# Performance work log

Measured on AMD Instinct MI355X. Metric: run time of the kernel, lower is better.

Reference implementation:

```python
import jax, jax.numpy as jnp
import numpy as np

B, IN_DIM, HID, ODE_STEPS = 8192, 1024, 1024, 6
DT = 1.0


def setup_inputs() -> dict:
    key = jax.random.key(0)
    ks = jax.random.split(key, 8)
    s = 0.02  # init scale for stability
    return {
        "x": jax.random.normal(ks[0], (B, IN_DIM), dtype=jnp.float32),
        "h": jax.random.normal(ks[1], (B, HID), dtype=jnp.float32),
        "log_tau": jnp.zeros((HID,), dtype=jnp.float32),
        "W_in_w": jax.random.normal(ks[2], (HID, IN_DIM), dtype=jnp.float32) * s,
        "W_in_b": jnp.zeros((HID,), dtype=jnp.float32),
        "W_rec_w": jax.random.normal(ks[3], (HID, HID), dtype=jnp.float32) * s,
        "W_gate_w": jax.random.normal(ks[4], (HID, IN_DIM + HID), dtype=jnp.float32) * s,
        "W_gate_b": jnp.zeros((HID,), dtype=jnp.float32),
    }


def reference(x, h, log_tau, W_in_w, W_in_b, W_rec_w, W_gate_w, W_gate_b):
    # torch Linear: y = x @ W.T + b, W:(out,in)
    tau = jnp.exp(log_tau)                      # (HID,)
    input_drive = x @ W_in_w.T + W_in_b         # (B,HID), loop-invariant
    # W_gate acts on concat([x, h]); split into x-block and h-block.
    Wg_x = W_gate_w[:, :IN_DIM]
    Wg_h = W_gate_w[:, IN_DIM:]
    gate_x = x @ Wg_x.T + W_gate_b              # (B,HID), loop-invariant
    sub_dt = DT / ODE_STEPS
    scale = sub_dt / tau                        # (HID,)

    def step(h, _):
        gate = jax.nn.sigmoid(gate_x + h @ Wg_h.T)
        f = -h + gate * jnp.tanh(input_drive + h @ W_rec_w.T)
        return h + scale * f, None

    h, _ = jax.lax.scan(step, h, None, length=ODE_STEPS)
    return (h, h)
```

## Files before the change

### kernel.cpp

```cpp
#include <hip/hip_runtime.h>
#include <hip/hip_bf16.h>
#include <stdint.h>

#define B_DIM 8192
#define IN_DIMC 1024
#define HIDC 1024
#define K_DIM 1024
#define ODE_STEPS 6

typedef float f32x4 __attribute__((ext_vector_type(4)));
typedef short bf16x8 __attribute__((ext_vector_type(8)));
typedef unsigned short u16x8 __attribute__((ext_vector_type(8)));

__device__ __forceinline__ float bf2f(unsigned short u) {
    union { unsigned int u; float f; } c; c.u = ((unsigned int)u) << 16; return c.f;
}
__device__ __forceinline__ unsigned short f2bf(float f) {
    union { float f; unsigned int u; } c; c.f = f;
    unsigned int u = c.u;
    return (unsigned short)((u + 0x7fffu + ((u >> 16) & 1u)) >> 16);
}
__device__ __forceinline__ float fast_tanh(float x) {
    float e = __expf(2.0f * x);
    return 1.0f - 2.0f / (e + 1.0f);
}

constexpr size_t XN    = (size_t)B_DIM * IN_DIMC;
constexpr size_t HN    = (size_t)B_DIM * HIDC;
constexpr size_t WINN  = (size_t)HIDC * IN_DIMC;
constexpr size_t WRECN = (size_t)HIDC * HIDC;
constexpr size_t WGN   = (size_t)HIDC * (IN_DIMC + HIDC);
constexpr size_t TOTQ  = (XN + HN + WINN + WRECN + WGN) / 4;

__global__ __launch_bounds__(256) void convert_all(
    const float* __restrict__ x, const float* __restrict__ h,
    const float* __restrict__ win, const float* __restrict__ wrec,
    const float* __restrict__ wgate,
    unsigned short* __restrict__ x_bf, unsigned short* __restrict__ h_bf,
    unsigned short* __restrict__ win_bf, unsigned short* __restrict__ wrec_bf,
    unsigned short* __restrict__ wgx_bf, unsigned short* __restrict__ wgh_bf)
{
    size_t q = (size_t)blockIdx.x * 256 + threadIdx.x;
    if (q >= TOTQ) return;
    size_t e = q * 4;
    const float* src; unsigned short* dst; size_t si, di;
    if (e < XN)                          { src = x;    si = e;                       dst = x_bf;    di = si; }
    else if (e < XN + HN)                { src = h;    si = e - XN;                  dst = h_bf;    di = si; }
    else if (e < XN + HN + WINN)         { src = win;  si = e - XN - HN;             dst = win_bf;  di = si; }
    else if (e < XN + HN + WINN + WRECN) { src = wrec; si = e - XN - HN - WINN;      dst = wrec_bf; di = si; }
    else {
        size_t i = e - XN - HN - WINN - WRECN;
        size_t row = i >> 11, col = i & 2047;
        src = wgate; si = i;
        if (col < 1024) { dst = wgx_bf; di = row * 1024 + col; }
        else            { dst = wgh_bf; di = row * 1024 + (col - 1024); }
    }
    float4 v = *(const float4*)(src + si);
    ushort4 o;
    o.x = f2bf(v.x); o.y = f2bf(v.y); o.z = f2bf(v.z); o.w = f2bf(v.w);
    *(ushort4*)(dst + di) = o;
}

constexpr int BM = 128, BN = 64, BK = 32;
constexpr int NT = HIDC / BN;

__device__ __forceinline__ void gload_lds16(const void* g, void* l) {
    __builtin_amdgcn_global_load_lds(
        (const __attribute__((address_space(1))) void*)g,
        (__attribute__((address_space(3))) void*)l, 16, 0, 0);
}

template<bool STEP>
__global__ __launch_bounds__(256, 3) void ltc_gemm(
    const unsigned short* __restrict__ A,
    const unsigned short* __restrict__ B1,
    const unsigned short* __restrict__ B2,
    const unsigned short* __restrict__ GXID,
    const float* __restrict__ h_init,
    float* __restrict__ h_nat,
    const float* __restrict__ log_tau,
    float* __restrict__ h_out,
    float* __restrict__ h_out2,
    unsigned short* __restrict__ hbf_out,
    const float* __restrict__ bias1, const float* __restrict__ bias2,
    unsigned short* __restrict__ GXID_out)
{
    __shared__ __attribute__((aligned(16))) unsigned short lA[BM * BK];
    __shared__ __attribute__((aligned(16))) unsigned short lB1[BN * BK];
    __shared__ __attribute__((aligned(16))) unsigned short lB2[BN * BK];

    const int tid = threadIdx.x;
    const int w = tid >> 6, l = tid & 63;
    const int mt = blockIdx.x / NT, nt = blockIdx.x % NT;
    const int m0 = mt * BM, n0 = nt * BN;
    const int wm = (w >> 1) * 64, wn = (w & 1) * 32;
    const int lrow = l >> 2, lcol = (l & 3) * 8;
    const int lm = l & 15, lq = l >> 4;

    f32x4 acc1[4][2], acc2[4][2];
    f32x4 z4 = {0.f, 0.f, 0.f, 0.f};
    #pragma unroll
    for (int i = 0; i < 4; i++)
        #pragma unroll
        for (int j = 0; j < 2; j++) { acc1[i][j] = z4; acc2[i][j] = z4; }

    const int arow = w * 32;
    const unsigned short* Bsrc = (w < 2) ? B1 : B2;
    unsigned short* lBdst = (w < 2) ? lB1 : lB2;
    const int brow = (w & 1) * 32;

    for (int k0 = 0; k0 < K_DIM; k0 += BK) {
        #pragma unroll
        for (int i = 0; i < 2; i++) {
            int ra = arow + i * 16;
            int rb = brow + i * 16;
            gload_lds16(A    + (size_t)(m0 + ra + lrow) * K_DIM + k0 + lcol, &lA[ra * BK]);
            gload_lds16(Bsrc + (size_t)(n0 + rb + lrow) * K_DIM + k0 + lcol, &lBdst[rb * BK]);
        }
        __syncthreads();

        bf16x8 af[4], f1[2], f2[2];
        #pragma unroll
        for (int mi = 0; mi < 4; mi++)
            af[mi] = *(const bf16x8*)&lA[(wm + mi * 16 + lm) * BK + lq * 8];
        #pragma unroll
        for (int ni = 0; ni < 2; ni++) {
            f1[ni] = *(const bf16x8*)&lB1[(wn + ni * 16 + lm) * BK + lq * 8];
            f2[ni] = *(const bf16x8*)&lB2[(wn + ni * 16 + lm) * BK + lq * 8];
        }
        #pragma unroll
        for (int mi = 0; mi < 4; mi++)
            #pragma unroll
            for (int ni = 0; ni < 2; ni++) {
                acc1[mi][ni] = __builtin_amdgcn_mfma_f32_16x16x32_bf16(af[mi], f1[ni], acc1[mi][ni], 0, 0, 0);
                acc2[mi][ni] = __builtin_amdgcn_mfma_f32_16x16x32_bf16(af[mi], f2[ni], acc2[mi][ni], 0, 0, 0);
            }
        __syncthreads();
    }

    constexpr float subdt = 1.0f / (float)ODE_STEPS;
    const size_t wslot = (((size_t)blockIdx.x * 4 + w) * 8) * 64 + l;

    #pragma unroll
    for (int mi = 0; mi < 4; mi++) {
        #pragma unroll
        for (int ni = 0; ni < 2; ni++) {
            const int gmb = m0 + wm + mi * 16 + lq * 4;
            const int gn  = n0 + wn + ni * 16 + lm;
            const size_t slot = wslot + (size_t)(mi * 2 + ni) * 64;
            if (STEP) {
                const float sc = subdt * __expf(-log_tau[gn]);
                u16x8 gi = *(const u16x8*)&GXID[slot * 8];
                f32x4 st;
                if (h_init) {
                    #pragma unroll
                    for (int r = 0; r < 4; r++)
                        st[r] = h_init[(size_t)(gmb + r) * HIDC + gn];
                } else {
                    st = *(const f32x4*)&h_nat[slot * 4];
                }
                f32x4 hn;
                #pragma unroll
                for (int r = 0; r < 4; r++) {
                    float gx = bf2f((unsigned short)gi[r])     + acc1[mi][ni][r];
                    float dr = bf2f((unsigned short)gi[4 + r]) + acc2[mi][ni][r];
                    float gt = fast_tanh(dr) / (1.0f + __expf(-gx));
                    hn[r] = fmaf(sc, gt - st[r], st[r]);
                }
                if (h_out) {
                    #pragma unroll
                    for (int r = 0; r < 4; r++) {
                        size_t idx = (size_t)(gmb + r) * HIDC + gn;
                        h_out[idx]  = hn[r];
                        h_out2[idx] = hn[r];
                    }
                } else {
                    *(f32x4*)&h_nat[slot * 4] = hn;
                    #pragma unroll
                    for (int r = 0; r < 4; r++)
                        hbf_out[(size_t)(gmb + r) * HIDC + gn] = f2bf(hn[r]);
                }
            } else {
                const float b1 = bias1[gn], b2 = bias2[gn];
                u16x8 o;
                #pragma unroll
                for (int r = 0; r < 4; r++) {
                    o[r]     = f2bf(acc1[mi][ni][r] + b1);
                    o[4 + r] = f2bf(acc2[mi][ni][r] + b2);
                }
                *(u16x8*)&GXID_out[slot * 8] = o;
            }
        }
    }
}

extern "C" void kernel_launch(void* const* d_in, const int* in_sizes, int n_in,
                              void* d_out, int out_size, void* d_ws, size_t ws_size,
                              hipStream_t stream)
{
    const float* x    = (const float*)d_in[0];
    const float* h    = (const float*)d_in[1];
    const float* ltau = (const float*)d_in[2];
    const float* winw = (const float*)d_in[3];
    const float* winb = (const float*)d_in[4];
    const float* wrec = (const float*)d_in[5];
    const float* wg   = (const float*)d_in[6];
    const float* wgb  = (const float*)d_in[7];

    char* ws = (char*)d_ws;
    unsigned short* x_bf    = (unsigned short*)ws; ws += XN * 2;
    unsigned short* h_bf0   = (unsigned short*)ws; ws += HN * 2;
    unsigned short* h_bf1   = (unsigned short*)ws; ws += HN * 2;
    unsigned short* win_bf  = (unsigned short*)ws; ws += WINN * 2;
    unsigned short* wrec_bf = (unsigned short*)ws; ws += WRECN * 2;
    unsigned short* wgx_bf  = (unsigned short*)ws; ws += WINN * 2;
    unsigned short* wgh_bf  = (unsigned short*)ws; ws += WRECN * 2;
    unsigned short* GXID    = (unsigned short*)ws; ws += HN * 2 * 2;
    float*          h_nat   = (float*)ws;          ws += HN * 4;

    float* hout  = (float*)d_out;
    float* hout2 = hout + (size_t)B_DIM * HIDC;

    convert_all<<<(int)(TOTQ / 256), 256, 0, stream>>>(
        x, h, winw, wrec, wg, x_bf, h_bf0, win_bf, wrec_bf, wgx_bf, wgh_bf);

    const int grid = (B_DIM / BM) * NT;
    ltc_gemm<false><<<grid, 256, 0, stream>>>(
        x_bf, wgx_bf, win_bf,
        nullptr, nullptr, nullptr, nullptr, nullptr, nullptr, nullptr,
        wgb, winb, GXID);

    unsigned short* hbf[2] = {h_bf0, h_bf1};
    for (int s = 0; s < ODE_STEPS; s++) {
        const bool last = (s == ODE_STEPS - 1);
        ltc_gemm<true><<<grid, 256, 0, stream>>>(
            hbf[s & 1], wgh_bf, wrec_bf,
            GXID,
            (s == 0) ? h : nullptr,
            h_nat, ltau,
            last ? hout : nullptr, last ? hout2 : nullptr,
            last ? nullptr : hbf[(s + 1) & 1],
            nullptr, nullptr, nullptr);
    }
}
```

Measured before the change: 520.1 us.

## Widen GEMM tile to 128x128, double-buffer LDS, and remap blocks across XCDs

Doubles the N tile so each workgroup computes a 128x128 output for both fused GEMMs, which halves the A-tile reloads per output. Adds a two-stage LDS buffer so the next K slice is fetched while the current one is multiplied. Remaps block IDs so each group of eight consecutive launched blocks is spread across the grid, aimed at better L2 locality across XCDs. Per-column constants are hoisted out of the epilogue. The cost is double the accumulator registers and LDS, with launch bounds lowered to two waves, which reduces occupancy.

```diff
diff --git a/kernel.cpp b/kernel.cpp
--- a/kernel.cpp
+++ b/kernel.cpp
@@ -61,8 +61,9 @@
     *(ushort4*)(dst + di) = o;
 }
 
-constexpr int BM = 128, BN = 64, BK = 32;
+constexpr int BM = 128, BN = 128, BK = 32;
 constexpr int NT = HIDC / BN;
+constexpr int GRID = (B_DIM / BM) * NT;
 
 __device__ __forceinline__ void gload_lds16(const void* g, void* l) {
     __builtin_amdgcn_global_load_lds(
@@ -71,7 +72,7 @@
 }
 
 template<bool STEP>
-__global__ __launch_bounds__(256, 3) void ltc_gemm(
+__global__ __launch_bounds__(256, 2) void ltc_gemm(
     const unsigned short* __restrict__ A,
     const unsigned short* __restrict__ B1,
     const unsigned short* __restrict__ B2,
@@ -85,71 +86,91 @@
     const float* __restrict__ bias1, const float* __restrict__ bias2,
     unsigned short* __restrict__ GXID_out)
 {
-    __shared__ __attribute__((aligned(16))) unsigned short lA[BM * BK];
-    __shared__ __attribute__((aligned(16))) unsigned short lB1[BN * BK];
-    __shared__ __attribute__((aligned(16))) unsigned short lB2[BN * BK];
+    __shared__ __attribute__((aligned(16))) unsigned short lA [2][BM * BK];
+    __shared__ __attribute__((aligned(16))) unsigned short lB1[2][BN * BK];
+    __shared__ __attribute__((aligned(16))) unsigned short lB2[2][BN * BK];
 
     const int tid = threadIdx.x;
     const int w = tid >> 6, l = tid & 63;
-    const int mt = blockIdx.x / NT, nt = blockIdx.x % NT;
+    const int bid = (blockIdx.x & 7) * (GRID / 8) + (blockIdx.x >> 3);
+    const int mt = bid / NT, nt = bid % NT;
     const int m0 = mt * BM, n0 = nt * BN;
-    const int wm = (w >> 1) * 64, wn = (w & 1) * 32;
+    const int wm = (w >> 1) * 64, wn = (w & 1) * 64;
     const int lrow = l >> 2, lcol = (l & 3) * 8;
     const int lm = l & 15, lq = l >> 4;
 
-    f32x4 acc1[4][2], acc2[4][2];
+    f32x4 acc1[4][4], acc2[4][4];
     f32x4 z4 = {0.f, 0.f, 0.f, 0.f};
     #pragma unroll
     for (int i = 0; i < 4; i++)
         #pragma unroll
-        for (int j = 0; j < 2; j++) { acc1[i][j] = z4; acc2[i][j] = z4; }
-
-    const int arow = w * 32;
-    const unsigned short* Bsrc = (w < 2) ? B1 : B2;
-    unsigned short* lBdst = (w < 2) ? lB1 : lB2;
-    const int brow = (w & 1) * 32;
-
+        for (int j = 0; j < 4; j++) { acc1[i][j] = z4; acc2[i][j] = z4; }
+
+    const int srow = w * 32 + lrow;
+    const unsigned short* gA  = A  + (size_t)(m0 + srow) * K_DIM + lcol;
+    const unsigned short* gB1 = B1 + (size_t)(n0 + srow) * K_DIM + lcol;
+    const unsigned short* gB2 = B2 + (size_t)(n0 + srow) * K_DIM + lcol;
+    const int lo = (w * 32) * BK;
+
+    auto STAGE = [&](int buf, int k0) {
+        gload_lds16(gA  + k0,               &lA [buf][lo]);
+        gload_lds16(gA  + 16 * K_DIM + k0,  &lA [buf][lo + 16 * BK]);
+        gload_lds16(gB1 + k0,               &lB1[buf][lo]);
+        gload_lds16(gB1 + 16 * K_DIM + k0,  &lB1[buf][lo + 16 * BK]);
+        gload_lds16(gB2 + k0,               &lB2[buf][lo]);
+        gload_lds16(gB2 + 16 * K_DIM + k0,  &lB2[buf][lo + 16 * BK]);
+    };
+
+    STAGE(0, 0);
+    __syncthreads();
+    int cur = 0;
     for (int k0 = 0; k0 < K_DIM; k0 += BK) {
-        #pragma unroll
-        for (int i = 0; i < 2; i++) {
-            int ra = arow + i * 16;
-            int rb = brow + i * 16;
-            gload_lds16(A    + (size_t)(m0 + ra + lrow) * K_DIM + k0 + lcol, &lA[ra * BK]);
-            gload_lds16(Bsrc + (size_t)(n0 + rb + lrow) * K_DIM + k0 + lcol, &lBdst[rb * BK]);
-        }
-        __syncthreads();
-
-        bf16x8 af[4], f1[2], f2[2];
+        if (k0 + BK < K_DIM) STAGE(cur ^ 1, k0 + BK);
+
+        bf16x8 af[4], f1[4], f2[4];
         #pragma unroll
         for (int mi = 0; mi < 4; mi++)
-            af[mi] = *(const bf16x8*)&lA[(wm + mi * 16 + lm) * BK + lq * 8];
-        #pragma unroll
-        for (int ni = 0; ni < 2; ni++) {
-            f1[ni] = *(const bf16x8*)&lB1[(wn + ni * 16 + lm) * BK + lq * 8];
-            f2[ni] = *(const bf16x8*)&lB2[(wn + ni * 16 + lm) * BK + lq * 8];
+            af[mi] = *(const bf16x8*)&lA[cur][(wm + mi * 16 + lm) * BK + lq * 8];
+        #pragma unroll
+        for (int ni = 0; ni < 4; ni++) {
+            f1[ni] = *(const bf16x8*)&lB1[cur][(wn + ni * 16 + lm) * BK + lq * 8];
+            f2[ni] = *(const bf16x8*)&lB2[cur][(wn + ni * 16 + lm) * BK + lq * 8];
         }
         #pragma unroll
         for (int mi = 0; mi < 4; mi++)
             #pragma unroll
-            for (int ni = 0; ni < 2; ni++) {
+            for (int ni = 0; ni < 4; ni++) {
                 acc1[mi][ni] = __builtin_amdgcn_mfma_f32_16x16x32_bf16(af[mi], f1[ni], acc1[mi][ni], 0, 0, 0);
                 acc2[mi][ni] = __builtin_amdgcn_mfma_f32_16x16x32_bf16(af[mi], f2[ni], acc2[mi][ni], 0, 0, 0);
             }
         __syncthreads();
+        cur ^= 1;
     }
 
     constexpr float subdt = 1.0f / (float)ODE_STEPS;
-    const size_t wslot = (((size_t)blockIdx.x * 4 + w) * 8) * 64 + l;
+    const size_t wslot = (((size_t)bid * 4 + w) * 16) * 64 + l;
+
+    float pc1[4], pc2[4];
+    #pragma unroll
+    for (int ni = 0; ni < 4; ni++) {
+        const int gn = n0 + wn + ni * 16 + lm;
+        if (STEP) {
+            pc1[ni] = subdt * __expf(-log_tau[gn]);
+        } else {
+            pc1[ni] = bias1[gn];
+            pc2[ni] = bias2[gn];
+        }
+    }
 
     #pragma unroll
     for (int mi = 0; mi < 4; mi++) {
         #pragma unroll
-        for (int ni = 0; ni < 2; ni++) {
+        for (int ni = 0; ni < 4; ni++) {
             const int gmb = m0 + wm + mi * 16 + lq * 4;
             const int gn  = n0 + wn + ni * 16 + lm;
-            const size_t slot = wslot + (size_t)(mi * 2 + ni) * 64;
+            const size_t slot = wslot + (size_t)(mi * 4 + ni) * 64;
             if (STEP) {
-                const float sc = subdt * __expf(-log_tau[gn]);
+                const float sc = pc1[ni];
                 u16x8 gi = *(const u16x8*)&GXID[slot * 8];
                 f32x4 st;
                 if (h_init) {
@@ -181,12 +202,11 @@
                         hbf_out[(size_t)(gmb + r) * HIDC + gn] = f2bf(hn[r]);
                 }
             } else {
-                const float b1 = bias1[gn], b2 = bias2[gn];
                 u16x8 o;
                 #pragma unroll
                 for (int r = 0; r < 4; r++) {
-                    o[r]     = f2bf(acc1[mi][ni][r] + b1);
-                    o[4 + r] = f2bf(acc2[mi][ni][r] + b2);
+                    o[r]     = f2bf(acc1[mi][ni][r] + pc1[ni]);
+                    o[4 + r] = f2bf(acc2[mi][ni][r] + pc2[ni]);
                 }
                 *(u16x8*)&GXID_out[slot * 8] = o;
             }
@@ -224,8 +244,7 @@
     convert_all<<<(int)(TOTQ / 256), 256, 0, stream>>>(
         x, h, winw, wrec, wg, x_bf, h_bf0, win_bf, wrec_bf, wgx_bf, wgh_bf);
 
-    const int grid = (B_DIM / BM) * NT;
-    ltc_gemm<false><<<grid, 256, 0, stream>>>(
+    ltc_gemm<false><<<GRID, 256, 0, stream>>>(
         x_bf, wgx_bf, win_bf,
         nullptr, nullptr, nullptr, nullptr, nullptr, nullptr, nullptr,
         wgb, winb, GXID);
@@ -233,7 +252,7 @@
     unsigned short* hbf[2] = {h_bf0, h_bf1};
     for (int s = 0; s < ODE_STEPS; s++) {
         const bool last = (s == ODE_STEPS - 1);
-        ltc_gemm<true><<<grid, 256, 0, stream>>>(
+        ltc_gemm<true><<<GRID, 256, 0, stream>>>(
             hbf[s & 1], wgh_bf, wrec_bf,
             GXID,
             (s == 0) ? h : nullptr,
```

Result: faster. 500.3 us (-3.8%).
